# Kernel optimization log

Measured on AMD Instinct MI355X. Metric: run time of the kernel, lower is better.

## Reference

```python
import jax, jax.numpy as jnp
import numpy as np
import math

D_MODEL = 1024
MEM_SIZE = 4096
N_HEADS = 8
BATCH = 4
SEQ = 1024
TOP_K = min(SEQ, MEM_SIZE // 10)  # 409, matches torch: min(seq_len, memory_size//10)
UPDATE_RATE = 0.01


def _gelu(x):
    return jax.nn.gelu(x, approximate=False)  # torch nn.GELU default (erf)


def setup_inputs() -> dict:
    key = jax.random.key(0)
    ks = jax.random.split(key, 26)
    w = lambda k, shape, s=0.02: (jax.random.normal(k, shape, jnp.float32) * s)
    inp = {
        "x": jax.random.normal(ks[0], (BATCH, SEQ, D_MODEL), jnp.float32),
        "memory_bank": jax.random.normal(ks[1], (MEM_SIZE, D_MODEL), jnp.float32) * 0.1,
        "memory_indices": jax.random.randint(ks[2], (BATCH, TOP_K), 0, MEM_SIZE, jnp.int32),
        # memory_encoder: Linear -> GELU -> Linear
        "enc_w1": w(ks[3], (D_MODEL, D_MODEL)), "enc_b1": jnp.zeros((D_MODEL,), jnp.float32),
        "enc_w2": w(ks[4], (D_MODEL, D_MODEL)), "enc_b2": jnp.zeros((D_MODEL,), jnp.float32),
        # MultiheadAttention in/out projections
        "wq": w(ks[5], (D_MODEL, D_MODEL)), "bq": jnp.zeros((D_MODEL,), jnp.float32),
        "wk": w(ks[6], (D_MODEL, D_MODEL)), "bk": jnp.zeros((D_MODEL,), jnp.float32),
        "wv": w(ks[7], (D_MODEL, D_MODEL)), "bv": jnp.zeros((D_MODEL,), jnp.float32),
        "wo": w(ks[8], (D_MODEL, D_MODEL)), "bo": jnp.zeros((D_MODEL,), jnp.float32),
        # memory_decoder: Linear -> GELU -> Linear
        "dec_w1": w(ks[9], (D_MODEL, D_MODEL)), "dec_b1": jnp.zeros((D_MODEL,), jnp.float32),
        "dec_w2": w(ks[10], (D_MODEL, D_MODEL)), "dec_b2": jnp.zeros((D_MODEL,), jnp.float32),
        # LayerNorm
        "ln_g": jnp.ones((D_MODEL,), jnp.float32), "ln_b": jnp.zeros((D_MODEL,), jnp.float32),
        # importance_scorer: Linear(d,64) -> GELU -> Linear(64,1) -> Sigmoid
        "imp_w1": w(ks[11], (D_MODEL, 64)), "imp_b1": jnp.zeros((64,), jnp.float32),
        "imp_w2": w(ks[12], (64, 1)), "imp_b2": jnp.zeros((1,), jnp.float32),
    }
    return inp


def reference(x, memory_bank, memory_indices,
              enc_w1, enc_b1, enc_w2, enc_b2,
              wq, bq, wk, bk, wv, bv, wo, bo,
              dec_w1, dec_b1, dec_w2, dec_b2,
              ln_g, ln_b, imp_w1, imp_b1, imp_w2, imp_b2):
    B, L, D = x.shape
    M = memory_bank.shape[0]
    H = N_HEADS
    dh = D // H

    # memory_encoder (dropout inactive at eval)
    enc = _gelu(x @ enc_w1 + enc_b1) @ enc_w2 + enc_b2  # [B,L,D]

    # cross-attention: query = encoded input, key/value = memory bank (shared across batch)
    q = (enc @ wq + bq).reshape(B, L, H, dh)
    k = (memory_bank @ wk + bk).reshape(M, H, dh)
    v = (memory_bank @ wv + bv).reshape(M, H, dh)
    scores = jnp.einsum('blhd,mhd->bhlm', q, k) * (1.0 / math.sqrt(dh))
    attn = jax.nn.softmax(scores, axis=-1)                 # [B,H,L,M]
    ctx = jnp.einsum('bhlm,mhd->blhd', attn, v).reshape(B, L, D)
    mem_out = ctx @ wo + bo

    # memory_decoder + residual + LayerNorm
    dec = _gelu(mem_out @ dec_w1 + dec_b1) @ dec_w2 + dec_b2
    comb = x + dec
    mu = jnp.mean(comb, axis=-1, keepdims=True)
    var = jnp.var(comb, axis=-1, keepdims=True)
    out = (comb - mu) / jnp.sqrt(var + 1e-5) * ln_g + ln_b  # [B,L,D]

    # _update_memory: importance top-k select + sequential EMA scatter into memory bank
    imp = jax.nn.sigmoid(_gelu(x @ imp_w1 + imp_b1) @ imp_w2 + imp_b2)[..., 0]  # [B,L]
    _, top_idx = jax.lax.top_k(imp, TOP_K)                  # [B,K]
    top_tok = jnp.take_along_axis(x, top_idx[..., None], axis=1)  # [B,K,D]

    # faithful to the torch double loop (b outer, k inner): sequential EMA with
    # chained updates on index collisions
    flat_idx = memory_indices.reshape(-1)
    flat_tok = top_tok.reshape(-1, D)

    def body(mem, xs):
        i, t = xs
        row = (1.0 - UPDATE_RATE) * mem[i] + UPDATE_RATE * t
        return mem.at[i].set(row), None

    new_mem, _ = jax.lax.scan(body, memory_bank, (flat_idx, flat_tok))
    return out, new_mem
```

## Files before the change

kernel.cpp:

```cpp
#include <hip/hip_runtime.h>

typedef unsigned short u16;
typedef __attribute__((ext_vector_type(4))) int i4;
typedef __attribute__((ext_vector_type(4))) unsigned u4;
typedef __attribute__((ext_vector_type(4))) unsigned short us4;
typedef __attribute__((ext_vector_type(8))) short short8;
typedef __attribute__((ext_vector_type(4))) float f4;

#define D_MODEL 1024
#define ROWS 4096
#define NHEAD 8
#define DH 128
#define TOPK 409
#define NUPD 1636
#define NBATCH 4
#define MAXC 64
#define ATTNROWS 32768

__device__ __forceinline__ u16 f2bf(float f) {
  unsigned u = __builtin_bit_cast(unsigned, f);
  u += 0x7fffu + ((u >> 16) & 1u);
  return (u16)(u >> 16);
}
__device__ __forceinline__ float bf2f(u16 b) {
  unsigned u = ((unsigned)b) << 16;
  return __builtin_bit_cast(float, u);
}
__device__ __forceinline__ float gelu_f(float v) {
  return 0.5f * v * (1.0f + erff(v * 0.70710678118654752f));
}
__device__ __forceinline__ void gload16(const void* g, void* l) {
  __builtin_amdgcn_global_load_lds((const __attribute__((address_space(1))) void*)g,
                                   (__attribute__((address_space(3))) void*)l, 16, 0, 0);
}

__global__ __launch_bounds__(256) void conv_kernel(const float* __restrict__ in,
                                                   u16* __restrict__ out, int n4) {
  int i = blockIdx.x * 256 + threadIdx.x;
  if (i < n4) {
    f4 v = ((const f4*)in)[i];
    us4 o;
    o.x = f2bf(v.x); o.y = f2bf(v.y); o.z = f2bf(v.z); o.w = f2bf(v.w);
    ((us4*)out)[i] = o;
  }
}

__global__ __launch_bounds__(256) void wtrans8_kernel(const float* s0, const float* s1,
                                                      const float* s2, const float* s3,
                                                      const float* s4, const float* s5,
                                                      const float* s6, const float* s7,
                                                      u16* __restrict__ dst) {
  const float* srcs[8] = {s0, s1, s2, s3, s4, s5, s6, s7};
  const float* w = srcs[blockIdx.z];
  u16* wt = dst + (size_t)blockIdx.z * (1024 * 1024);
  __shared__ float t[32][33];
  int tx = threadIdx.x & 31, ty = threadIdx.x >> 5;
  int k0 = blockIdx.y * 32, n0 = blockIdx.x * 32;
  for (int r = 0; r < 4; ++r)
    t[ty + r * 8][tx] = w[(size_t)(k0 + ty + r * 8) * 1024 + n0 + tx];
  __syncthreads();
  for (int r = 0; r < 4; ++r)
    wt[(size_t)(n0 + ty + r * 8) * 1024 + k0 + tx] = f2bf(t[tx][ty + r * 8]);
}

__global__ __launch_bounds__(256) void bias_prep_kernel(const float* __restrict__ b2,
                                                        const float* __restrict__ wq,
                                                        const float* __restrict__ bq,
                                                        const float* __restrict__ bo,
                                                        const float* __restrict__ dw1,
                                                        const float* __restrict__ db1,
                                                        float* __restrict__ bqp,
                                                        float* __restrict__ bodp) {
  int id = blockIdx.x;
  int n = (id & 3) * 256 + threadIdx.x;
  const float* bvec = (id < 4) ? b2 : bo;
  const float* W = (id < 4) ? wq : dw1;
  const float* badd = (id < 4) ? bq : db1;
  float* out = (id < 4) ? bqp : bodp;
  float s = 0.0f;
  for (int k = 0; k < 1024; ++k) s += bvec[k] * W[(size_t)k * 1024 + n];
  out[n] = s + badd[n];
}

__global__ __launch_bounds__(256) void gemm_sq(const u16* __restrict__ A0,
                                               const u16* __restrict__ B0,
                                               u16* __restrict__ C0,
                                               const u16* __restrict__ A1,
                                               const u16* __restrict__ B1,
                                               u16* __restrict__ C1) {
  __shared__ __align__(16) char al[2 * 128 * 64];
  __shared__ __align__(16) char bl[2 * 64 * 64];
  const int K = 1024, N = 1024;
  const int id = blockIdx.x;
  const int which = id >> 7, j = id & 127;
  const u16* A = which ? A1 : A0;
  const u16* BT = which ? B1 : B0;
  u16* C = which ? C1 : C0;
  const int m0 = (j >> 4) * 128, n0 = (j & 15) * 64;
  const int tid = threadIdx.x;
  const int lane = tid & 63, wid = tid >> 6;
  const int g = lane >> 4, qi = lane & 15;
  const int wr = wid >> 1, wc = wid & 1;
  f4 acc[4][2] = {};

  const int a0r = tid >> 2, a0b = (tid & 3) ^ ((a0r >> 1) & 3);
  const int c1 = tid + 256;
  const int a1r = c1 >> 2, a1b = (c1 & 3) ^ ((a1r >> 1) & 3);
  const int b0r = tid >> 2, b0b = (tid & 3) ^ ((b0r >> 1) & 3);

#define STAGE(buf, kt)                                                                   \
  {                                                                                      \
    const int k0_ = (kt) * 32;                                                           \
    gload16(A + (size_t)(m0 + a0r) * K + k0_ + a0b * 8, al + (buf) * 8192 + tid * 16);   \
    gload16(A + (size_t)(m0 + a1r) * K + k0_ + a1b * 8, al + (buf) * 8192 + c1 * 16);    \
    gload16(BT + (size_t)(n0 + b0r) * K + k0_ + b0b * 8, bl + (buf) * 4096 + tid * 16);  \
  }

  STAGE(0, 0);
  __syncthreads();
  int cur = 0;
  for (int kt = 0; kt < 32; ++kt) {
    if (kt + 1 < 32) STAGE(cur ^ 1, kt + 1);
    short8 af[4], bfr[2];
    for (int i = 0; i < 4; ++i) {
      int r = wr * 64 + i * 16 + qi;
      af[i] = *(const short8*)(al + cur * 8192 + r * 64 + ((g ^ ((r >> 1) & 3))) * 16);
    }
    for (int sn = 0; sn < 2; ++sn) {
      int r = wc * 32 + sn * 16 + qi;
      bfr[sn] = *(const short8*)(bl + cur * 4096 + r * 64 + ((g ^ ((r >> 1) & 3))) * 16);
    }
    for (int i = 0; i < 4; ++i)
      for (int sn = 0; sn < 2; ++sn)
        acc[i][sn] = __builtin_amdgcn_mfma_f32_16x16x32_bf16(af[i], bfr[sn], acc[i][sn], 0, 0, 0);
    __syncthreads();
    cur ^= 1;
  }
#undef STAGE

  for (int i = 0; i < 4; ++i) {
    int row = m0 + wr * 64 + i * 16 + g * 4;
    for (int sn = 0; sn < 2; ++sn) {
      int col = n0 + wc * 32 + sn * 16 + qi;
      for (int jj = 0; jj < 4; ++jj)
        C[(size_t)(row + jj) * N + col] = f2bf(acc[i][sn][jj]);
    }
  }
}

template <int EPI>
__global__ __launch_bounds__(256) void gemm_bt(const u16* __restrict__ A,
                                               const u16* __restrict__ BT,
                                               const float* __restrict__ bias,
                                               void* __restrict__ C) {
  __shared__ __align__(16) char al[2 * 128 * 64];
  __shared__ __align__(16) char bl[2 * 64 * 64];
  const int K = 1024, N = 1024;
  const int id = blockIdx.x;
  const int xcd = id & 7, j = id >> 3;
  const int m0 = ((j & 3) * 8 + xcd) * 128;
  const int n0 = (j >> 2) * 64;
  const int tid = threadIdx.x;
  const int lane = tid & 63, wid = tid >> 6;
  const int g = lane >> 4, qi = lane & 15;
  const int wr = wid >> 1, wc = wid & 1;
  f4 acc[4][2] = {};

  const int a0r = tid >> 2, a0b = (tid & 3) ^ ((a0r >> 1) & 3);
  const int c1 = tid + 256;
  const int a1r = c1 >> 2, a1b = (c1 & 3) ^ ((a1r >> 1) & 3);
  const int b0r = tid >> 2, b0b = (tid & 3) ^ ((b0r >> 1) & 3);

#define STAGE(buf, kt)                                                                   \
  {                                                                                      \
    const int k0_ = (kt) * 32;                                                           \
    gload16(A + (size_t)(m0 + a0r) * K + k0_ + a0b * 8, al + (buf) * 8192 + tid * 16);   \
    gload16(A + (size_t)(m0 + a1r) * K + k0_ + a1b * 8, al + (buf) * 8192 + c1 * 16);    \
    gload16(BT + (size_t)(n0 + b0r) * K + k0_ + b0b * 8, bl + (buf) * 4096 + tid * 16);  \
  }

  STAGE(0, 0);
  __syncthreads();
  int cur = 0;
  for (int kt = 0; kt < 32; ++kt) {
    if (kt + 1 < 32) STAGE(cur ^ 1, kt + 1);
    short8 af[4], bfr[2];
    for (int i = 0; i < 4; ++i) {
      int r = wr * 64 + i * 16 + qi;
      af[i] = *(const short8*)(al + cur * 8192 + r * 64 + ((g ^ ((r >> 1) & 3))) * 16);
    }
    for (int sn = 0; sn < 2; ++sn) {
      int r = wc * 32 + sn * 16 + qi;
      bfr[sn] = *(const short8*)(bl + cur * 4096 + r * 64 + ((g ^ ((r >> 1) & 3))) * 16);
    }
    for (int i = 0; i < 4; ++i)
      for (int sn = 0; sn < 2; ++sn)
        acc[i][sn] = __builtin_amdgcn_mfma_f32_16x16x32_bf16(af[i], bfr[sn], acc[i][sn], 0, 0, 0);
    __syncthreads();
    cur ^= 1;
  }
#undef STAGE

  for (int i = 0; i < 4; ++i) {
    int row = m0 + wr * 64 + i * 16 + g * 4;
    for (int sn = 0; sn < 2; ++sn) {
      int col = n0 + wc * 32 + sn * 16 + qi;
      float bv = bias[col];
      for (int jj = 0; jj < 4; ++jj) {
        float v = acc[i][sn][jj] + bv;
        if constexpr (EPI == 1) v = gelu_f(v);
        if constexpr (EPI == 2)
          ((float*)C)[(size_t)(row + jj) * N + col] = v;
        else
          ((u16*)C)[(size_t)(row + jj) * N + col] = f2bf(v);
      }
    }
  }
}

__global__ __launch_bounds__(256) void gemm_kv(const u16* __restrict__ A,
                                               const u16* __restrict__ BT,
                                               const float* __restrict__ bk,
                                               const float* __restrict__ bv,
                                               u16* __restrict__ Ck, u16* __restrict__ CvT) {
  __shared__ __align__(16) char pool[2 * 128 * 64 + 2 * 64 * 64];
  char* al = pool;
  char* bl = pool + 2 * 128 * 64;
  const int id = blockIdx.x;
  const int xcd = id & 7, j = id >> 3;
  const int m0 = ((j & 3) * 8 + xcd) * 128;
  const int n0 = (j >> 2) * 64;
  const int tid = threadIdx.x;
  const int lane = tid & 63, wid = tid >> 6;
  const int g = lane >> 4, qi = lane & 15;
  const int wr = wid >> 1, wc = wid & 1;
  const int K = 1024, M = 4096;
  f4 acc[4][2] = {};

  const int a0r = tid >> 2, a0b = (tid & 3) ^ ((a0r >> 1) & 3);
  const int c1 = tid + 256;
  const int a1r = c1 >> 2, a1b = (c1 & 3) ^ ((a1r >> 1) & 3);
  const int b0r = tid >> 2, b0b = (tid & 3) ^ ((b0r >> 1) & 3);

#define STAGE(buf, kt)                                                                   \
  {                                                                                      \
    const int k0_ = (kt) * 32;                                                           \
    gload16(A + (size_t)(m0 + a0r) * K + k0_ + a0b * 8, al + (buf) * 8192 + tid * 16);   \
    gload16(A + (size_t)(m0 + a1r) * K + k0_ + a1b * 8, al + (buf) * 8192 + c1 * 16);    \
    gload16(BT + (size_t)(n0 + b0r) * K + k0_ + b0b * 8, bl + (buf) * 4096 + tid * 16);  \
  }

  STAGE(0, 0);
  __syncthreads();
  int cur = 0;
  for (int kt = 0; kt < 32; ++kt) {
    if (kt + 1 < 32) STAGE(cur ^ 1, kt + 1);
    short8 af[4], bfr[2];
    for (int i = 0; i < 4; ++i) {
      int r = wr * 64 + i * 16 + qi;
      af[i] = *(const short8*)(al + cur * 8192 + r * 64 + ((g ^ ((r >> 1) & 3))) * 16);
    }
    for (int sn = 0; sn < 2; ++sn) {
      int r = wc * 32 + sn * 16 + qi;
      bfr[sn] = *(const short8*)(bl + cur * 4096 + r * 64 + ((g ^ ((r >> 1) & 3))) * 16);
    }
    for (int i = 0; i < 4; ++i)
      for (int sn = 0; sn < 2; ++sn)
        acc[i][sn] = __builtin_amdgcn_mfma_f32_16x16x32_bf16(af[i], bfr[sn], acc[i][sn], 0, 0, 0);
    __syncthreads();
    cur ^= 1;
  }
#undef STAGE

  if (n0 < 1024) {
    for (int i = 0; i < 4; ++i) {
      int row = m0 + wr * 64 + i * 16 + g * 4;
      for (int sn = 0; sn < 2; ++sn) {
        int col = n0 + wc * 32 + sn * 16 + qi;
        float bvv = bk[col];
        for (int jj = 0; jj < 4; ++jj)
          Ck[(size_t)(row + jj) * 1024 + col] = f2bf(acc[i][sn][jj] + bvv);
      }
    }
  } else {
    u16(*t)[132] = (u16(*)[132])pool;
    __syncthreads();
    for (int i = 0; i < 4; ++i)
      for (int sn = 0; sn < 2; ++sn) {
        int nl = wc * 32 + sn * 16 + qi;
        float bvv = bv[n0 - 1024 + nl];
        for (int jj = 0; jj < 4; ++jj)
          t[nl][wr * 64 + i * 16 + g * 4 + jj] = f2bf(acc[i][sn][jj] + bvv);
      }
    __syncthreads();
    int r = tid >> 2, cg = tid & 3;
    for (int v = 0; v < 4; ++v) {
      us4 val = *(const us4*)&t[r][cg * 32 + v * 8];
      *(us4*)&CvT[(size_t)(n0 - 1024 + r) * M + m0 + cg * 32 + v * 8] = val;
    }
  }
}

template <int LP>
__global__ __launch_bounds__(512) void attn_kernel(const u16* __restrict__ q,
                                                   const u16* __restrict__ kp,
                                                   const u16* __restrict__ vT,
                                                   u16* __restrict__ cp0, u16* __restrict__ cp1,
                                                   u16* __restrict__ cp2, u16* __restrict__ cp3,
                                                   float* __restrict__ ml) {
  constexpr int MR = 4096 >> LP;
  constexpr int NT = MR / 64;
  __shared__ __align__(16) char kl[64 * 256];
  __shared__ __align__(16) char vl[128 * 128];
  const int id = blockIdx.x;
  const int h = id & 7;
  const int rest = id >> 3;
  const int part = rest & ((1 << LP) - 1);
  const int qblk = (rest >> LP) & 7;
  const int b = rest >> (3 + LP);
  const int tid = threadIdx.x;
  const int lane = tid & 63, wid = tid >> 6;
  const int g = lane >> 4, qi = lane & 15;
  const int qrow = b * 1024 + qblk * 128 + wid * 16 + qi;
  const float scale = 0.08838834764831845f;
  u16* ctp = (part == 0) ? cp0 : (part == 1) ? cp1 : (part == 2) ? cp2 : cp3;

  short8 qf[4];
  for (int kk = 0; kk < 4; ++kk)
    qf[kk] = *(const short8*)(q + (size_t)qrow * 1024 + h * 128 + kk * 32 + g * 8);

  const int kc0 = tid, kc1 = tid + 512;
  const int kr0 = kc0 >> 4, kb0 = kc0 & 15, kr1 = kc1 >> 4, kb1 = kc1 & 15;
  const int vr0 = kc0 >> 3, vb0 = kc0 & 7, vr1 = kc1 >> 3, vb1 = kc1 & 7;
  const int kd0 = kr0 * 256 + (kb0 ^ (kr0 & 7)) * 16;
  const int kd1 = kr1 * 256 + (kb1 ^ (kr1 & 7)) * 16;
  const int vd0 = vr0 * 128 + (vb0 ^ (vr0 & 7)) * 16;
  const int vd1 = vr1 * 128 + (vb1 ^ (vr1 & 7)) * 16;
  const int mbase = part * MR;
  const u16* kg0 = kp + (size_t)kr0 * 1024 + h * 128 + kb0 * 8;
  const u16* kg1 = kp + (size_t)kr1 * 1024 + h * 128 + kb1 * 8;
  const u16* vg0 = vT + (size_t)(h * 128 + vr0) * 4096 + vb0 * 8;
  const u16* vg1 = vT + (size_t)(h * 128 + vr1) * 4096 + vb1 * 8;

  i4 kreg0, kreg1, vreg0, vreg1;
#define LOADREGS(mt_)                                  \
  {                                                    \
    const int m0_ = mbase + (mt_) * 64;                \
    kreg0 = *(const i4*)(kg0 + (size_t)m0_ * 1024);    \
    kreg1 = *(const i4*)(kg1 + (size_t)m0_ * 1024);    \
    vreg0 = *(const i4*)(vg0 + m0_);                   \
    vreg1 = *(const i4*)(vg1 + m0_);                   \
  }

  f4 ct[8] = {};
  float mrun = -1e30f, lsum = 0.0f;

  LOADREGS(0);
  for (int mt = 0; mt < NT; ++mt) {
    __syncthreads();
    *(i4*)(kl + kd0) = kreg0;
    *(i4*)(kl + kd1) = kreg1;
    *(i4*)(vl + vd0) = vreg0;
    *(i4*)(vl + vd1) = vreg1;
    __syncthreads();
    if (mt + 1 < NT) LOADREGS(mt + 1);

    f4 st[4] = {};
    for (int s = 0; s < 4; ++s) {
      int n = s * 16 + qi;
      const char* krow = kl + n * 256;
      int sw = n & 7;
      for (int kk = 0; kk < 4; ++kk) {
        short8 a = *(const short8*)(krow + ((kk * 4 + g) ^ sw) * 16);
        st[s] = __builtin_amdgcn_mfma_f32_16x16x32_bf16(a, qf[kk], st[s], 0, 0, 0);
      }
    }
    float sv[16];
    float tmax = -1e30f;
    for (int s = 0; s < 4; ++s)
      for (int jj = 0; jj < 4; ++jj) {
        float v = st[s][jj] * scale;
        sv[s * 4 + jj] = v;
        tmax = fmaxf(tmax, v);
      }
    tmax = fmaxf(tmax, __shfl_xor(tmax, 16, 64));
    tmax = fmaxf(tmax, __shfl_xor(tmax, 32, 64));
    float mnew = fmaxf(mrun, tmax);
    float r = __expf(mrun - mnew);
    float psum = 0.0f;
    for (int i = 0; i < 16; ++i) {
      sv[i] = __expf(sv[i] - mnew);
      psum += sv[i];
    }
    psum += __shfl_xor(psum, 16, 64);
    psum += __shfl_xor(psum, 32, 64);
    lsum = lsum * r + psum;
    mrun = mnew;
    for (int i = 0; i < 8; ++i) ct[i] = ct[i] * r;

    unsigned pk0[4], pk1[4];
    for (int s = 0; s < 4; ++s) {
      pk0[s] = (unsigned)f2bf(sv[s * 4 + 0]) | ((unsigned)f2bf(sv[s * 4 + 1]) << 16);
      pk1[s] = (unsigned)f2bf(sv[s * 4 + 2]) | ((unsigned)f2bf(sv[s * 4 + 3]) << 16);
    }
    const int src1 = qi + ((g & 1) << 5);
    const int src2 = src1 + 16;
    const bool hi = (g & 2) != 0;
    for (int p = 0; p < 2; ++p) {
      unsigned a0 = __shfl(pk0[2 * p], src1, 64), b0 = __shfl(pk0[2 * p + 1], src1, 64);
      unsigned a1 = __shfl(pk1[2 * p], src1, 64), b1 = __shfl(pk1[2 * p + 1], src1, 64);
      unsigned a2 = __shfl(pk0[2 * p], src2, 64), b2 = __shfl(pk0[2 * p + 1], src2, 64);
      unsigned a3 = __shfl(pk1[2 * p], src2, 64), b3 = __shfl(pk1[2 * p + 1], src2, 64);
      u4 bw;
      bw.x = hi ? b0 : a0; bw.y = hi ? b1 : a1; bw.z = hi ? b2 : a2; bw.w = hi ? b3 : a3;
      short8 pf = __builtin_bit_cast(short8, bw);
      for (int d = 0; d < 8; ++d) {
        int dr = d * 16 + qi;
        short8 a = *(const short8*)(vl + dr * 128 + (((p * 4 + g) ^ (dr & 7))) * 16);
        ct[d] = __builtin_amdgcn_mfma_f32_16x16x32_bf16(a, pf, ct[d], 0, 0, 0);
      }
    }
  }
#undef LOADREGS

  const int orow = ((b * 8 + h) << 10) + qblk * 128 + wid * 16 + qi;
  if (g == 0) {
    ml[(size_t)(part * ATTNROWS + orow) * 2 + 0] = mrun;
    ml[(size_t)(part * ATTNROWS + orow) * 2 + 1] = lsum;
  }
  for (int d = 0; d < 8; ++d) {
    us4 o;
    o.x = f2bf(ct[d][0]); o.y = f2bf(ct[d][1]);
    o.z = f2bf(ct[d][2]); o.w = f2bf(ct[d][3]);
    *(us4*)(ctp + (size_t)orow * 128 + d * 16 + g * 4) = o;
  }
}

__global__ __launch_bounds__(256) void combine4_kernel(const u16* __restrict__ cp0,
                                                       const u16* __restrict__ cp1,
                                                       const u16* __restrict__ cp2,
                                                       const u16* __restrict__ cp3,
                                                       const float* __restrict__ ml,
                                                       u16* __restrict__ ctx) {
  int tid = threadIdx.x;
  int row = blockIdx.x * 16 + (tid >> 4);
  int dp = (tid & 15) * 8;
  float m0 = ml[(size_t)row * 2], l0 = ml[(size_t)row * 2 + 1];
  float m1 = ml[((size_t)ATTNROWS + row) * 2], l1 = ml[((size_t)ATTNROWS + row) * 2 + 1];
  float m2 = ml[((size_t)2 * ATTNROWS + row) * 2], l2 = ml[((size_t)2 * ATTNROWS + row) * 2 + 1];
  float m3 = ml[((size_t)3 * ATTNROWS + row) * 2], l3 = ml[((size_t)3 * ATTNROWS + row) * 2 + 1];
  float m = fmaxf(fmaxf(m0, m1), fmaxf(m2, m3));
  float s0 = __expf(m0 - m), s1 = __expf(m1 - m), s2 = __expf(m2 - m), s3 = __expf(m3 - m);
  float inv = 1.0f / (l0 * s0 + l1 * s1 + l2 * s2 + l3 * s3);
  short8 c0 = *(const short8*)(cp0 + (size_t)row * 128 + dp);
  short8 c1 = *(const short8*)(cp1 + (size_t)row * 128 + dp);
  short8 c2 = *(const short8*)(cp2 + (size_t)row * 128 + dp);
  short8 c3 = *(const short8*)(cp3 + (size_t)row * 128 + dp);
  us4 o[2];
  for (int i = 0; i < 8; ++i) {
    float f = (bf2f((u16)c0[i]) * s0 + bf2f((u16)c1[i]) * s1 + bf2f((u16)c2[i]) * s2 +
               bf2f((u16)c3[i]) * s3) * inv;
    ((u16*)o)[i] = f2bf(f);
  }
  int bb = row >> 13, hh = (row >> 10) & 7, qr = row & 1023;
  *(short8*)(ctx + (size_t)((bb << 10) + qr) * 1024 + hh * 128 + dp) =
      __builtin_bit_cast(short8, o);
}

__global__ __launch_bounds__(256) void ln_kernel(const float* __restrict__ x,
                                                 const float* __restrict__ dec,
                                                 const float* __restrict__ gw,
                                                 const float* __restrict__ bw,
                                                 float* __restrict__ out,
                                                 int* __restrict__ cnt) {
  __shared__ float rs[256], rs2[256];
  int row = blockIdx.x, tid = threadIdx.x;
  if (tid == 0) cnt[row] = 0;
  float c[4];
  float s = 0.0f, s2 = 0.0f;
  for (int i = 0; i < 4; ++i) {
    int col = tid + i * 256;
    float v = x[(size_t)row * 1024 + col] + dec[(size_t)row * 1024 + col];
    c[i] = v; s += v; s2 += v * v;
  }
  rs[tid] = s; rs2[tid] = s2;
  __syncthreads();
  for (int st = 128; st > 0; st >>= 1) {
    if (tid < st) { rs[tid] += rs[tid + st]; rs2[tid] += rs2[tid + st]; }
    __syncthreads();
  }
  float mu = rs[0] * (1.0f / 1024.0f);
  float var = rs2[0] * (1.0f / 1024.0f) - mu * mu;
  float inv = rsqrtf(var + 1e-5f);
  for (int i = 0; i < 4; ++i) {
    int col = tid + i * 256;
    out[(size_t)row * 1024 + col] = (c[i] - mu) * inv * gw[col] + bw[col];
  }
}

__global__ __launch_bounds__(256) void imp_kernel(const float* __restrict__ x,
                                                  const float* __restrict__ w1,
                                                  const float* __restrict__ b1,
                                                  const float* __restrict__ w2,
                                                  const float* __restrict__ b2,
                                                  float* __restrict__ imp) {
  __shared__ float xs[8][1024];
  int tid = threadIdx.x;
  int lane = tid & 63, wid = tid >> 6;
  size_t base = (size_t)blockIdx.x * 8192;
  for (int i = 0; i < 32; ++i) ((float*)xs)[tid + i * 256] = x[base + tid + i * 256];
  __syncthreads();
  int r0 = wid * 2, r1 = wid * 2 + 1;
  float a0 = 0.0f, a1 = 0.0f;
  for (int k = 0; k < 1024; ++k) {
    float wv = w1[k * 64 + lane];
    a0 += xs[r0][k] * wv;
    a1 += xs[r1][k] * wv;
  }
  float h0 = gelu_f(a0 + b1[lane]) * w2[lane];
  float h1 = gelu_f(a1 + b1[lane]) * w2[lane];
  for (int d = 1; d < 64; d <<= 1) {
    h0 += __shfl_xor(h0, d, 64);
    h1 += __shfl_xor(h1, d, 64);
  }
  if (lane == 0) {
    imp[blockIdx.x * 8 + r0] = 1.0f / (1.0f + expf(-(h0 + b2[0])));
    imp[blockIdx.x * 8 + r1] = 1.0f / (1.0f + expf(-(h1 + b2[0])));
  }
}

__global__ __launch_bounds__(512) void topk_kernel(const float* __restrict__ imp,
                                                   int* __restrict__ tidx) {
  __shared__ float v[1024];
  __shared__ int ix[1024];
  int b = blockIdx.x, tid = threadIdx.x;
  for (int i = tid; i < 1024; i += 512) { v[i] = imp[b * 1024 + i]; ix[i] = i; }
  __syncthreads();
  for (int k = 2; k <= 1024; k <<= 1) {
    for (int j = k >> 1; j > 0; j >>= 1) {
      for (int t = tid; t < 1024; t += 512) {
        int p = t ^ j;
        if (p > t) {
          float va = v[t], vb = v[p];
          int ia = ix[t], ib = ix[p];
          bool ord = (va > vb) || (va == vb && ia < ib);
          bool up = ((t & k) == 0);
          if (up ? !ord : ord) { v[t] = vb; v[p] = va; ix[t] = ib; ix[p] = ia; }
        }
      }
      __syncthreads();
    }
  }
  for (int t = tid; t < TOPK; t += 512) tidx[b * TOPK + t] = ix[t];
}

__global__ __launch_bounds__(128) void rank_kernel(const int* __restrict__ midx,
                                                   int* __restrict__ cnt,
                                                   int* __restrict__ slot) {
  __shared__ int mi[NUPD];
  int tid = threadIdx.x;
  for (int i = tid; i < NUPD; i += 128) mi[i] = midx[i];
  __syncthreads();
  int j = blockIdx.x * 128 + tid;
  if (j < NUPD) {
    int r = mi[j], rank = 0;
    for (int jp = 0; jp < j; ++jp) rank += (mi[jp] == r) ? 1 : 0;
    if (rank < MAXC) slot[r * MAXC + rank] = j;
    atomicAdd(&cnt[r], 1);
  }
}

__global__ __launch_bounds__(256) void apply_kernel(const float* __restrict__ x,
                                                    const float* __restrict__ mem,
                                                    const int* __restrict__ tidx,
                                                    const int* __restrict__ cnt,
                                                    const int* __restrict__ slot,
                                                    float* __restrict__ outm) {
  int row = blockIdx.x, tid = threadIdx.x;
  f4 acc = ((const f4*)(mem + (size_t)row * 1024))[tid];
  int c = cnt[row];
  c = c < MAXC ? c : MAXC;
  for (int t = 0; t < c; ++t) {
    int j = slot[row * MAXC + t];
    int b = j / TOPK;
    int tr = tidx[j];
    f4 xv = ((const f4*)(x + ((size_t)b * 1024 + tr) * 1024))[tid];
    acc = acc * 0.99f + xv * 0.01f;
  }
  ((f4*)(outm + (size_t)row * 1024))[tid] = acc;
}

extern "C" void kernel_launch(void* const* d_in, const int* in_sizes, int n_in,
                              void* d_out, int out_size, void* d_ws, size_t ws_size,
                              hipStream_t stream) {
  const float* x = (const float*)d_in[0];
  const float* memory_bank = (const float*)d_in[1];
  const int* memory_indices = (const int*)d_in[2];
  const float* enc_w1 = (const float*)d_in[3];
  const float* enc_b1 = (const float*)d_in[4];
  const float* enc_w2 = (const float*)d_in[5];
  const float* enc_b2 = (const float*)d_in[6];
  const float* wq = (const float*)d_in[7];
  const float* bq = (const float*)d_in[8];
  const float* wk = (const float*)d_in[9];
  const float* bk = (const float*)d_in[10];
  const float* wv = (const float*)d_in[11];
  const float* bv = (const float*)d_in[12];
  const float* wo = (const float*)d_in[13];
  const float* bo = (const float*)d_in[14];
  const float* dec_w1 = (const float*)d_in[15];
  const float* dec_b1 = (const float*)d_in[16];
  const float* dec_w2 = (const float*)d_in[17];
  const float* dec_b2 = (const float*)d_in[18];
  const float* ln_g = (const float*)d_in[19];
  const float* ln_b = (const float*)d_in[20];
  const float* imp_w1 = (const float*)d_in[21];
  const float* imp_b1 = (const float*)d_in[22];
  const float* imp_w2 = (const float*)d_in[23];
  const float* imp_b2 = (const float*)d_in[24];

  char* ws = (char*)d_ws;
  u16* buf0 = (u16*)(ws);
  u16* buf1 = (u16*)(ws + (8ull << 20));
  u16* buf2 = (u16*)(ws + (16ull << 20));
  u16* buf3 = (u16*)(ws + (24ull << 20));
  u16* buf4 = (u16*)(ws + (32ull << 20));
  float* decb = (float*)(ws + (40ull << 20));
  u16* wtb = (u16*)(ws + (56ull << 20));
  float* impb = (float*)(ws + (72ull << 20));
  int* tidx = (int*)(ws + (72ull << 20) + (1 << 16));
  float* bqp = (float*)(ws + (72ull << 20) + (1 << 17));
  float* bodp = (float*)(ws + (72ull << 20) + (1 << 17) + 4096);
  int* cnt = (int*)buf3;
  int* slot = (int*)(ws + (24ull << 20) + (1 << 16));
  u16* w2n = (u16*)(ws + (40ull << 20));
  u16* won = (u16*)(ws + (42ull << 20));
  u16* cp0 = buf1;
  u16* cp1 = buf2;
  u16* cp2 = (u16*)(ws + (40ull << 20));
  u16* cp3 = (u16*)(ws + (48ull << 20));
  float* ml = (float*)(ws + (56ull << 20));

  const int NM = 1024 * 1024;
  u16* wt_e1 = wtb + 0 * NM;
  u16* wt_e2q = wtb + 1 * NM;
  u16* wt_q = wtb + 2 * NM;
  u16* wt_k = wtb + 3 * NM;
  u16* wt_od = wtb + 5 * NM;
  u16* wt_d1 = wtb + 6 * NM;
  u16* wt_d2 = wtb + 7 * NM;

  conv_kernel<<<4096, 256, 0, stream>>>(x, buf0, ROWS * D_MODEL / 4);
  conv_kernel<<<4096, 256, 0, stream>>>(memory_bank, buf2, ROWS * D_MODEL / 4);
  wtrans8_kernel<<<dim3(32, 32, 8), 256, 0, stream>>>(enc_w1, enc_w2, wq, wk, wv, wo,
                                                      dec_w1, dec_w2, wtb);
  conv_kernel<<<1024, 256, 0, stream>>>(enc_w2, w2n, NM / 4);
  conv_kernel<<<1024, 256, 0, stream>>>(wo, won, NM / 4);

  gemm_sq<<<256, 256, 0, stream>>>(wt_q, w2n, wt_e2q, wt_d1, won, wt_od);
  bias_prep_kernel<<<8, 256, 0, stream>>>(enc_b2, wq, bq, bo, dec_w1, dec_b1, bqp, bodp);

  gemm_bt<1><<<512, 256, 0, stream>>>(buf0, wt_e1, enc_b1, buf1);
  gemm_bt<0><<<512, 256, 0, stream>>>(buf1, wt_e2q, bqp, buf0);
  gemm_kv<<<1024, 256, 0, stream>>>(buf2, wt_k, bk, bv, buf3, buf4);

  attn_kernel<2><<<1024, 512, 0, stream>>>(buf0, buf3, buf4, cp0, cp1, cp2, cp3, ml);
  combine4_kernel<<<2048, 256, 0, stream>>>(cp0, cp1, cp2, cp3, ml, buf0);

  gemm_bt<1><<<512, 256, 0, stream>>>(buf0, wt_od, bodp, buf1);
  gemm_bt<2><<<512, 256, 0, stream>>>(buf1, wt_d2, dec_b2, decb);
  ln_kernel<<<4096, 256, 0, stream>>>(x, decb, ln_g, ln_b, (float*)d_out, cnt);

  imp_kernel<<<512, 256, 0, stream>>>(x, imp_w1, imp_b1, imp_w2, imp_b2, impb);
  topk_kernel<<<NBATCH, 512, 0, stream>>>(impb, tidx);
  rank_kernel<<<13, 128, 0, stream>>>(memory_indices, cnt, slot);
  apply_kernel<<<4096, 256, 0, stream>>>(x, memory_bank, tidx, cnt, slot,
                                         (float*)d_out + (size_t)ROWS * D_MODEL);
}
```

Baseline: 455.2 us.

## Double-buffer attention K/V tiles via direct global-to-LDS loads; merge small launches

The attention kernel now stages K and V tiles with global_load_lds into two LDS buffers, prefetching the next tile while computing the current one. This drops the register round-trip and one barrier per iteration, but doubles LDS use to 64KB per block, which may lower occupancy. The conversion kernels are also merged into paired launches. The serial bias-prep reduction is split across 64 blocks plus a small final reduction to expose more parallelism.

```diff
diff --git a/kernel.cpp b/kernel.cpp
--- a/kernel.cpp
+++ b/kernel.cpp
@@ -34,15 +34,18 @@
                                    (__attribute__((address_space(3))) void*)l, 16, 0, 0);
 }
 
-__global__ __launch_bounds__(256) void conv_kernel(const float* __restrict__ in,
-                                                   u16* __restrict__ out, int n4) {
-  int i = blockIdx.x * 256 + threadIdx.x;
-  if (i < n4) {
-    f4 v = ((const f4*)in)[i];
-    us4 o;
-    o.x = f2bf(v.x); o.y = f2bf(v.y); o.z = f2bf(v.z); o.w = f2bf(v.w);
-    ((us4*)out)[i] = o;
-  }
+__global__ __launch_bounds__(256) void conv2_kernel(const float* __restrict__ in0,
+                                                    u16* __restrict__ out0,
+                                                    const float* __restrict__ in1,
+                                                    u16* __restrict__ out1, int nb) {
+  int bid = blockIdx.x;
+  const float* in = (bid < nb) ? in0 : in1;
+  u16* out = (bid < nb) ? out0 : out1;
+  int i = (bid < nb ? bid : bid - nb) * 256 + threadIdx.x;
+  f4 v = ((const f4*)in)[i];
+  us4 o;
+  o.x = f2bf(v.x); o.y = f2bf(v.y); o.z = f2bf(v.z); o.w = f2bf(v.w);
+  ((us4*)out)[i] = o;
 }
 
 __global__ __launch_bounds__(256) void wtrans8_kernel(const float* s0, const float* s1,
@@ -63,22 +66,34 @@
     wt[(size_t)(n0 + ty + r * 8) * 1024 + k0 + tx] = f2bf(t[tx][ty + r * 8]);
 }
 
-__global__ __launch_bounds__(256) void bias_prep_kernel(const float* __restrict__ b2,
-                                                        const float* __restrict__ wq,
-                                                        const float* __restrict__ bq,
-                                                        const float* __restrict__ bo,
-                                                        const float* __restrict__ dw1,
-                                                        const float* __restrict__ db1,
-                                                        float* __restrict__ bqp,
-                                                        float* __restrict__ bodp) {
+__global__ __launch_bounds__(256) void bias_partA(const float* __restrict__ b2,
+                                                  const float* __restrict__ wq,
+                                                  const float* __restrict__ bo,
+                                                  const float* __restrict__ dw1,
+                                                  float* __restrict__ pbuf) {
   int id = blockIdx.x;
+  int which = id >> 5;
+  int kb = (id >> 2) & 7;
   int n = (id & 3) * 256 + threadIdx.x;
-  const float* bvec = (id < 4) ? b2 : bo;
-  const float* W = (id < 4) ? wq : dw1;
-  const float* badd = (id < 4) ? bq : db1;
-  float* out = (id < 4) ? bqp : bodp;
+  const float* bvec = which ? bo : b2;
+  const float* W = which ? dw1 : wq;
   float s = 0.0f;
-  for (int k = 0; k < 1024; ++k) s += bvec[k] * W[(size_t)k * 1024 + n];
+  for (int k = kb * 128; k < kb * 128 + 128; ++k) s += bvec[k] * W[(size_t)k * 1024 + n];
+  pbuf[(size_t)(which * 8 + kb) * 1024 + n] = s;
+}
+
+__global__ __launch_bounds__(256) void bias_partB(const float* __restrict__ pbuf,
+                                                  const float* __restrict__ bq,
+                                                  const float* __restrict__ db1,
+                                                  float* __restrict__ bqp,
+                                                  float* __restrict__ bodp) {
+  int id = blockIdx.x;
+  int which = id >> 2;
+  int n = (id & 3) * 256 + threadIdx.x;
+  float s = 0.0f;
+  for (int kb = 0; kb < 8; ++kb) s += pbuf[(size_t)(which * 8 + kb) * 1024 + n];
+  float* out = which ? bodp : bqp;
+  const float* badd = which ? db1 : bq;
   out[n] = s + badd[n];
 }
 
@@ -310,8 +325,8 @@
                                                    float* __restrict__ ml) {
   constexpr int MR = 4096 >> LP;
   constexpr int NT = MR / 64;
-  __shared__ __align__(16) char kl[64 * 256];
-  __shared__ __align__(16) char vl[128 * 128];
+  __shared__ __align__(16) char kl[2][16384];
+  __shared__ __align__(16) char vl[2][16384];
   const int id = blockIdx.x;
   const int h = id & 7;
   const int rest = id >> 3;
@@ -329,46 +344,39 @@
   for (int kk = 0; kk < 4; ++kk)
     qf[kk] = *(const short8*)(q + (size_t)qrow * 1024 + h * 128 + kk * 32 + g * 8);
 
-  const int kc0 = tid, kc1 = tid + 512;
-  const int kr0 = kc0 >> 4, kb0 = kc0 & 15, kr1 = kc1 >> 4, kb1 = kc1 & 15;
-  const int vr0 = kc0 >> 3, vb0 = kc0 & 7, vr1 = kc1 >> 3, vb1 = kc1 & 7;
-  const int kd0 = kr0 * 256 + (kb0 ^ (kr0 & 7)) * 16;
-  const int kd1 = kr1 * 256 + (kb1 ^ (kr1 & 7)) * 16;
-  const int vd0 = vr0 * 128 + (vb0 ^ (vr0 & 7)) * 16;
-  const int vd1 = vr1 * 128 + (vb1 ^ (vr1 & 7)) * 16;
   const int mbase = part * MR;
-  const u16* kg0 = kp + (size_t)kr0 * 1024 + h * 128 + kb0 * 8;
-  const u16* kg1 = kp + (size_t)kr1 * 1024 + h * 128 + kb1 * 8;
-  const u16* vg0 = vT + (size_t)(h * 128 + vr0) * 4096 + vb0 * 8;
-  const u16* vg1 = vT + (size_t)(h * 128 + vr1) * 4096 + vb1 * 8;
-
-  i4 kreg0, kreg1, vreg0, vreg1;
-#define LOADREGS(mt_)                                  \
-  {                                                    \
-    const int m0_ = mbase + (mt_) * 64;                \
-    kreg0 = *(const i4*)(kg0 + (size_t)m0_ * 1024);    \
-    kreg1 = *(const i4*)(kg1 + (size_t)m0_ * 1024);    \
-    vreg0 = *(const i4*)(vg0 + m0_);                   \
-    vreg1 = *(const i4*)(vg1 + m0_);                   \
+  const int kr0 = tid >> 4, kb0 = (tid & 15) ^ (kr0 & 7);
+  const int c1 = tid + 512;
+  const int kr1 = c1 >> 4, kb1 = (c1 & 15) ^ (kr1 & 7);
+  const int vr0 = tid >> 3, vb0 = (tid & 7) ^ (vr0 & 7);
+  const int vr1 = c1 >> 3, vb1 = (c1 & 7) ^ (vr1 & 7);
+  const u16* kg0 = kp + (size_t)(mbase + kr0) * 1024 + h * 128 + kb0 * 8;
+  const u16* kg1 = kp + (size_t)(mbase + kr1) * 1024 + h * 128 + kb1 * 8;
+  const u16* vg0 = vT + (size_t)(h * 128 + vr0) * 4096 + mbase + vb0 * 8;
+  const u16* vg1 = vT + (size_t)(h * 128 + vr1) * 4096 + mbase + vb1 * 8;
+
+#define STAGE(bi, mt_)                                      \
+  {                                                         \
+    const int o_ = (mt_) * 64;                              \
+    gload16(kg0 + (size_t)o_ * 1024, kl[bi] + tid * 16);    \
+    gload16(kg1 + (size_t)o_ * 1024, kl[bi] + c1 * 16);     \
+    gload16(vg0 + o_, vl[bi] + tid * 16);                   \
+    gload16(vg1 + o_, vl[bi] + c1 * 16);                    \
   }
 
   f4 ct[8] = {};
   float mrun = -1e30f, lsum = 0.0f;
 
-  LOADREGS(0);
+  STAGE(0, 0);
+  __syncthreads();
+  int cur = 0;
   for (int mt = 0; mt < NT; ++mt) {
-    __syncthreads();
-    *(i4*)(kl + kd0) = kreg0;
-    *(i4*)(kl + kd1) = kreg1;
-    *(i4*)(vl + vd0) = vreg0;
-    *(i4*)(vl + vd1) = vreg1;
-    __syncthreads();
-    if (mt + 1 < NT) LOADREGS(mt + 1);
+    if (mt + 1 < NT) STAGE(cur ^ 1, mt + 1);
 
     f4 st[4] = {};
     for (int s = 0; s < 4; ++s) {
       int n = s * 16 + qi;
-      const char* krow = kl + n * 256;
+      const char* krow = kl[cur] + n * 256;
       int sw = n & 7;
       for (int kk = 0; kk < 4; ++kk) {
         short8 a = *(const short8*)(krow + ((kk * 4 + g) ^ sw) * 16);
@@ -416,12 +424,14 @@
       short8 pf = __builtin_bit_cast(short8, bw);
       for (int d = 0; d < 8; ++d) {
         int dr = d * 16 + qi;
-        short8 a = *(const short8*)(vl + dr * 128 + (((p * 4 + g) ^ (dr & 7))) * 16);
+        short8 a = *(const short8*)(vl[cur] + dr * 128 + (((p * 4 + g) ^ (dr & 7))) * 16);
         ct[d] = __builtin_amdgcn_mfma_f32_16x16x32_bf16(a, pf, ct[d], 0, 0, 0);
       }
     }
-  }
-#undef LOADREGS
+    __syncthreads();
+    cur ^= 1;
+  }
+#undef STAGE
 
   const int orow = ((b * 8 + h) << 10) + qblk * 128 + wid * 16 + qi;
   if (g == 0) {
@@ -631,6 +641,7 @@
   int* tidx = (int*)(ws + (72ull << 20) + (1 << 16));
   float* bqp = (float*)(ws + (72ull << 20) + (1 << 17));
   float* bodp = (float*)(ws + (72ull << 20) + (1 << 17) + 4096);
+  float* pbuf = (float*)(ws + (72ull << 20) + 196608);
   int* cnt = (int*)buf3;
   int* slot = (int*)(ws + (24ull << 20) + (1 << 16));
   u16* w2n = (u16*)(ws + (40ull << 20));
@@ -650,15 +661,14 @@
   u16* wt_d1 = wtb + 6 * NM;
   u16* wt_d2 = wtb + 7 * NM;
 
-  conv_kernel<<<4096, 256, 0, stream>>>(x, buf0, ROWS * D_MODEL / 4);
-  conv_kernel<<<4096, 256, 0, stream>>>(memory_bank, buf2, ROWS * D_MODEL / 4);
+  conv2_kernel<<<8192, 256, 0, stream>>>(x, buf0, memory_bank, buf2, 4096);
   wtrans8_kernel<<<dim3(32, 32, 8), 256, 0, stream>>>(enc_w1, enc_w2, wq, wk, wv, wo,
                                                       dec_w1, dec_w2, wtb);
-  conv_kernel<<<1024, 256, 0, stream>>>(enc_w2, w2n, NM / 4);
-  conv_kernel<<<1024, 256, 0, stream>>>(wo, won, NM / 4);
+  conv2_kernel<<<2048, 256, 0, stream>>>(enc_w2, w2n, wo, won, 1024);
 
   gemm_sq<<<256, 256, 0, stream>>>(wt_q, w2n, wt_e2q, wt_d1, won, wt_od);
-  bias_prep_kernel<<<8, 256, 0, stream>>>(enc_b2, wq, bq, bo, dec_w1, dec_b1, bqp, bodp);
+  bias_partA<<<64, 256, 0, stream>>>(enc_b2, wq, bo, dec_w1, pbuf);
+  bias_partB<<<8, 256, 0, stream>>>(pbuf, bq, dec_b1, bqp, bodp);
 
   gemm_bt<1><<<512, 256, 0, stream>>>(buf0, wt_e1, enc_b1, buf1);
   gemm_bt<0><<<512, 256, 0, stream>>>(buf1, wt_e2q, bqp, buf0);
```

New measurement: 434.2 us. 1.05x faster.
